# Kernel optimization log

Measured on AMD Instinct MI355X. Metric: run time of the kernel, lower is better.

Reference implementation:

```python
import jax, jax.numpy as jnp
import numpy as np

L, C, K, D = 100000, 20000, 10000, 64   # learners, courses, concepts, feat dim (post-MLP 64)
E_UC, E_UK, E_CK = 1_500_000, 2_000_000, 200_000
LAYERS = 2
EPS = 1e-8


def _sym_laplace_bipartite(key, n_a, n_b, n_edges):
    """Random bipartite graph -> symmetric (n_a+n_b) COO with Laplace normalization,
    matching laplace_transform(): 1/(sqrt(rowsum)+eps) * A * 1/(sqrt(colsum)+eps)."""
    ka, kb = jax.random.split(key)
    a = jax.random.randint(ka, (n_edges,), 0, n_a)
    b = jax.random.randint(kb, (n_edges,), 0, n_b)
    ones = jnp.ones((n_edges,), jnp.float32)
    deg_a = jax.ops.segment_sum(ones, a, num_segments=n_a)
    deg_b = jax.ops.segment_sum(ones, b, num_segments=n_b)
    v = 1.0 / (jnp.sqrt(deg_a[a]) + EPS) / (jnp.sqrt(deg_b[b]) + EPS)
    rows = jnp.concatenate([a, b + n_a]).astype(jnp.int32)
    cols = jnp.concatenate([b + n_a, a]).astype(jnp.int32)
    vals = jnp.concatenate([v, v]).astype(jnp.float32)
    return rows, cols, vals


def setup_inputs() -> dict:
    key = jax.random.key(0)
    k1, k2, k3, k4, k5, k6 = jax.random.split(key, 6)
    cg_rows, cg_cols, cg_vals = _sym_laplace_bipartite(k1, L, C, E_UC)
    kg_rows, kg_cols, kg_vals = _sym_laplace_bipartite(k2, L, K, E_UK)
    # course-concept aggregation graph: row-normalized diag(1/(rowsum+eps)) @ G
    kc, kk = jax.random.split(k3)
    c = jax.random.randint(kc, (E_CK,), 0, C)
    k_ = jax.random.randint(kk, (E_CK,), 0, K)
    deg_c = jax.ops.segment_sum(jnp.ones((E_CK,), jnp.float32), c, num_segments=C)
    ca_vals = (1.0 / (deg_c + EPS))[c].astype(jnp.float32)
    return {
        "learners_feature": jax.random.normal(k4, (L, D), jnp.float32),
        "courses_feature": jax.random.normal(k5, (C, D), jnp.float32),
        "concepts_feature": jax.random.normal(k6, (K, D), jnp.float32),
        "cg_rows": cg_rows, "cg_cols": cg_cols, "cg_vals": cg_vals,
        "kg_rows": kg_rows, "kg_cols": kg_cols, "kg_vals": kg_vals,
        "ca_rows": c.astype(jnp.int32), "ca_cols": k_.astype(jnp.int32), "ca_vals": ca_vals,
    }


def _spmm(rows, cols, vals, feat, n_out):
    # sparse COO (n_out x n_in) @ dense (n_in x D): gather + weighted scatter-add
    return jax.ops.segment_sum(vals[:, None] * feat[cols], rows, num_segments=n_out)


def _l2norm(x):
    # F.normalize(p=2, dim=1) with eps clamp
    n = jnp.linalg.norm(x, axis=1, keepdims=True)
    return x / jnp.maximum(n, 1e-12)


def _graph_propagate(rows, cols, vals, A, B):
    feat = jnp.concatenate([A, B], axis=0)
    n = feat.shape[0]
    acc = feat  # layer-0 features (un-normalized, as in original all_features[0])
    for i in range(LAYERS):
        feat = _spmm(rows, cols, vals, feat, n) / (i + 2)
        acc = acc + _l2norm(feat)
    return acc[: A.shape[0]], acc[A.shape[0]:]


def reference(learners_feature, courses_feature, concepts_feature,
              cg_rows, cg_cols, cg_vals,
              kg_rows, kg_cols, kg_vals,
              ca_rows, ca_cols, ca_vals):
    # course-grained view: propagate over learner-course graph
    cg_l, cg_c = _graph_propagate(cg_rows, cg_cols, cg_vals, learners_feature, courses_feature)
    # concept-grained view: propagate over learner-concept graph
    kg_l, kg_k = _graph_propagate(kg_rows, kg_cols, kg_vals, learners_feature, concepts_feature)
    # aggregate concept-grained concept features into course representations
    kg_c = _spmm(ca_rows, ca_cols, ca_vals, kg_k, courses_feature.shape[0])
    learners_rep = cg_l + kg_l            # [L, D]
    courses_rep = cg_c + kg_c             # [C, D]
    return jnp.concatenate([learners_rep, courses_rep], axis=0)  # [L+C, D]
```

## Files before the change

### kernel.cpp

```cpp
#include <hip/hip_runtime.h>

#define D 64
#define S0 10
#define BCHUNK 8

#define BKT_CNTCG 0
#define BKT_CNTKG 256
#define BKT_BASECG 512
#define BKT_BASEKG 772
#define BKT_CURCG 1032
#define BKT_CURKG 1288
#define BKT_WORDS 2048

__device__ __forceinline__ unsigned int f2bf(float x) {
  unsigned int u = __float_as_uint(x);
  return (u + 0x7FFFu + ((u >> 16) & 1u)) >> 16;
}


__global__ __launch_bounds__(256) void axcopy_kernel(float* __restrict__ dst,
                                                     const float* __restrict__ src,
                                                     long long n4, float s) {
  long long i = (long long)blockIdx.x * blockDim.x + threadIdx.x;
  long long stride = (long long)gridDim.x * blockDim.x;
  for (; i < n4; i += stride) {
    float4 v = ((const float4*)src)[i];
    v.x *= s; v.y *= s; v.z *= s; v.w *= s;
    ((float4*)dst)[i] = v;
  }
}


__global__ __launch_bounds__(1024) void bincnt_kernel(
    const int* __restrict__ cgr, const int* __restrict__ cgc, long long EcgH,
    const int* __restrict__ kgr, const int* __restrict__ kgc, long long EkgH,
    const int* __restrict__ car, long long Eca,
    int* __restrict__ bkt, int* __restrict__ cadeg,
    int L, int NB0, int s1cg, int s1kg) {
  __shared__ int h[512];
  int t = threadIdx.x;
  if (t < 512) h[t] = 0;
  __syncthreads();
  long long i = (long long)blockIdx.x * blockDim.x + t;
  long long stride = (long long)gridDim.x * blockDim.x;
  long long t01 = EcgH + EkgH, tot = t01 + Eca;
  for (; i < tot; i += stride) {
    if (i < EcgH) {
      int a = cgr[i], c = cgc[i];
      atomicAdd(&h[a >> S0], 1);
      atomicAdd(&h[NB0 + ((c - L) >> s1cg)], 1);
    } else if (i < t01) {
      long long j = i - EcgH;
      int a = kgr[j], c = kgc[j];
      atomicAdd(&h[256 + (a >> S0)], 1);
      atomicAdd(&h[256 + NB0 + ((c - L) >> s1kg)], 1);
    } else {
      long long j = i - t01;
      atomicAdd(&cadeg[car[j]], 1);
    }
  }
  __syncthreads();
  if (t < 512 && h[t]) atomicAdd(&bkt[t], h[t]);
}

__global__ __launch_bounds__(256) void bktscan_kernel(int* __restrict__ bkt,
                                                      int NBcg, int NBkg) {
  __shared__ int lds[256];
  int t = threadIdx.x;
  #pragma unroll
  for (int g = 0; g < 2; ++g) {
    int NB      = g ? NBkg : NBcg;
    int cntoff  = g ? BKT_CNTKG : BKT_CNTCG;
    int baseoff = g ? BKT_BASEKG : BKT_BASECG;
    int curoff  = g ? BKT_CURKG : BKT_CURCG;
    lds[t] = (t < NB) ? bkt[cntoff + t] : 0;
    __syncthreads();
    for (int off = 1; off < 256; off <<= 1) {
      int x = (t >= off) ? lds[t - off] : 0;
      __syncthreads();
      lds[t] += x;
      __syncthreads();
    }
    int excl = (t == 0) ? 0 : lds[t - 1];
    if (t < NB) { bkt[baseoff + t] = excl; bkt[curoff + t] = excl; }
    if (t == NB - 1) bkt[baseoff + NB] = lds[t];
    __syncthreads();
  }
}

__global__ __launch_bounds__(256) void ca_scan1_kernel(const int* __restrict__ deg,
                                                       int* __restrict__ rp,
                                                       float* __restrict__ scal,
                                                       int* __restrict__ part, int n) {
  __shared__ int lds[256];
  int b = blockIdx.x, t = threadIdx.x;
  int base = b * 1024 + t * 4;
  int v[4]; int s = 0;
  #pragma unroll
  for (int j = 0; j < 4; j++) {
    int idx = base + j;
    v[j] = (idx < n) ? deg[idx] : 0;
    if (idx < n) scal[idx] = 1.0f / ((float)v[j] + 1e-8f);
    s += v[j];
  }
  lds[t] = s;
  __syncthreads();
  for (int off = 1; off < 256; off <<= 1) {
    int x = (t >= off) ? lds[t - off] : 0;
    __syncthreads();
    lds[t] += x;
    __syncthreads();
  }
  int run = (t == 0) ? 0 : lds[t - 1];
  if (t == 255) part[b] = lds[255];
  #pragma unroll
  for (int j = 0; j < 4; j++) { int idx = base + j; if (idx < n) rp[idx] = run; run += v[j]; }
}

__global__ __launch_bounds__(256) void ca_scan2_kernel(int* __restrict__ part, int nb) {
  __shared__ int lds[256];
  int t = threadIdx.x;
  lds[t] = (t < nb) ? part[t] : 0;
  __syncthreads();
  for (int off = 1; off < 256; off <<= 1) {
    int x = (t >= off) ? lds[t - off] : 0;
    __syncthreads();
    lds[t] += x;
    __syncthreads();
  }
  if (t < nb) part[t] = (t == 0) ? 0 : lds[t - 1];
}

__global__ __launch_bounds__(256) void ca_scan3_kernel(int* __restrict__ rp,
                                                       const int* __restrict__ part,
                                                       int* __restrict__ cacur,
                                                       int n, int total) {
  int b = blockIdx.x, t = threadIdx.x;
  int add = part[b];
  int base = b * 1024 + t * 4;
  #pragma unroll
  for (int j = 0; j < 4; j++) {
    int idx = base + j;
    if (idx < n) { int f = rp[idx] + add; rp[idx] = f; cacur[idx] = f; }
  }
  if (b == 0 && t == 0) rp[n] = total;
}

__global__ __launch_bounds__(256) void bin_kernel(
    const int* __restrict__ rowsA, const int* __restrict__ colsA, long long E,
    int L, int s1, int NB0, int NBtot,
    int* __restrict__ gcur, int* __restrict__ binned) {
  __shared__ int cnt[256];
  __shared__ int gbase[256];
  int t = threadIdx.x;
  long long base = (long long)blockIdx.x * (256 * BCHUNK);
  cnt[t] = 0;
  __syncthreads();
  int av[BCHUNK], cv_[BCHUNK], l0[BCHUNK], l1[BCHUNK];
  #pragma unroll
  for (int k = 0; k < BCHUNK; k++) {
    long long i = base + (long long)k * 256 + t;
    bool ok = i < E;
    int a = ok ? rowsA[i] : 0;
    int c = ok ? colsA[i] : L;
    av[k] = a; cv_[k] = c;
    if (ok) {
      int b0 = a >> S0;
      int b1 = NB0 + ((c - L) >> s1);
      l0[k] = atomicAdd(&cnt[b0], 1);
      l1[k] = atomicAdd(&cnt[b1], 1);
    } else { l0[k] = 0; l1[k] = 0; }
  }
  __syncthreads();
  if (t < NBtot) gbase[t] = cnt[t] ? atomicAdd(&gcur[t], cnt[t]) : 0;
  __syncthreads();
  #pragma unroll
  for (int k = 0; k < BCHUNK; k++) {
    long long i = base + (long long)k * 256 + t;
    if (i < E) {
      int a = av[k], c = cv_[k];
      int b0 = a >> S0;
      int b1 = NB0 + ((c - L) >> s1);
      binned[gbase[b0] + l0[k]] = ((a & ((1 << S0) - 1)) << 17) | c;
      binned[gbase[b1] + l1[k]] = (((c - L) & ((1 << s1) - 1)) << 17) | a;
    }
  }
}

__global__ __launch_bounds__(1024) void fine2_kernel(
    const int* __restrict__ binned, const int* __restrict__ bktbase,
    int* __restrict__ rp, int* __restrict__ cvout, float* __restrict__ scal,
    int L, int sideEnd, int s1, int NB0, int nfull) {
  __shared__ int cnt[1 << S0];
  int b = blockIdx.x, t = threadIdx.x;
  int rowbase, rowend;
  if (b < NB0) { rowbase = b << S0; rowend = min(rowbase + (1 << S0), L); }
  else { int bb = b - NB0; rowbase = L + (bb << s1); rowend = min(rowbase + (1 << s1), sideEnd); }
  int nrows = rowend - rowbase;
  int base = bktbase[b], end = bktbase[b + 1];
  cnt[t] = 0;
  __syncthreads();
  for (int i = base + t; i < end; i += 1024) atomicAdd(&cnt[binned[i] >> 17], 1);
  __syncthreads();
  int deg = cnt[t];
  for (int off = 1; off < 1024; off <<= 1) {
    int x = (t >= off) ? cnt[t - off] : 0;
    __syncthreads();
    cnt[t] += x;
    __syncthreads();
  }
  int excl = (t == 0) ? 0 : cnt[t - 1];
  int pos = base + excl;
  __syncthreads();
  cnt[t] = pos;
  if (t < nrows) {
    rp[rowbase + t] = pos;
    scal[rowbase + t] = 1.0f / (sqrtf((float)deg) + 1e-8f);
  }
  if (b == gridDim.x - 1 && t == 0) rp[nfull] = end;
  __syncthreads();
  for (int i = base + t; i < end; i += 1024) {
    int w = binned[i];
    int p = atomicAdd(&cnt[w >> 17], 1);
    cvout[p] = w & 0x1FFFF;
  }
}

__global__ __launch_bounds__(256) void scatter_ca_kernel(
    const int* __restrict__ rows, const int* __restrict__ cols,
    int* __restrict__ rowcur, int* __restrict__ cv, long long ne) {
  long long e = (long long)blockIdx.x * blockDim.x + threadIdx.x;
  if (e >= ne) return;
  int p = atomicAdd(&rowcur[rows[e]], 1);
  cv[p] = cols[e];
}

__global__ __launch_bounds__(256) void cvt_all_kernel(
    const float* __restrict__ learners, const float* __restrict__ courses,
    const float* __restrict__ concepts, const float* __restrict__ scal,
    unsigned short* __restrict__ g0, int Lr, int Ncg, int Rtot) {
  long long q = (long long)blockIdx.x * blockDim.x + threadIdx.x;
  long long stride = (long long)gridDim.x * blockDim.x;
  long long nq = (long long)Rtot * 16;
  for (; q < nq; q += stride) {
    int row = (int)(q >> 4);
    int sub = ((int)q & 15) * 4;
    const float* src;
    if (row < Ncg) src = (row < Lr) ? learners + (long long)row * D
                                    : courses + (long long)(row - Lr) * D;
    else {
      int r = row - Ncg;
      src = (r < Lr) ? learners + (long long)r * D
                     : concepts + (long long)(r - Lr) * D;
    }
    float sg = scal[row];
    float4 v = *(const float4*)(src + sub);
    unsigned int lo = f2bf(v.x * sg) | (f2bf(v.y * sg) << 16);
    unsigned int hi = f2bf(v.z * sg) | (f2bf(v.w * sg) << 16);
    *(uint2*)(g0 + (long long)row * D + sub) = make_uint2(lo, hi);
  }
}

template <int MODE, int INITA, int INITB>
__global__ __launch_bounds__(256) void pull4_kernel(
    const int* __restrict__ rowptr, const int* __restrict__ cols,
    const unsigned short* __restrict__ gt, unsigned short* __restrict__ g1,
    const float* __restrict__ sigRow,
    float* __restrict__ accA, float* __restrict__ accB, int splitAcc,
    const float* __restrict__ i0A, const float* __restrict__ i0B, int i0Split,
    float i0ScaleA, float i0ScaleB, int nrows) {
  int row = blockIdx.x * 4 + (threadIdx.x >> 6);
  if (row >= nrows) return;
  int lane = threadIdx.x & 63;
  int sub = lane & 15;
  int grp = lane >> 4;
  int e0 = rowptr[row], e1 = rowptr[row + 1];
  float sx = 0.f, sy = 0.f, sz = 0.f, sw = 0.f;
  long long dimoff = (long long)(sub << 2);
  int e = e0;
  for (; e + 16 <= e1; e += 16) {
    int c0 = cols[e + grp];
    int c1 = cols[e + 4 + grp];
    int c2 = cols[e + 8 + grp];
    int c3 = cols[e + 12 + grp];
    uint2 v0 = *(const uint2*)(gt + ((long long)c0 << 6) + dimoff);
    uint2 v1 = *(const uint2*)(gt + ((long long)c1 << 6) + dimoff);
    uint2 v2 = *(const uint2*)(gt + ((long long)c2 << 6) + dimoff);
    uint2 v3 = *(const uint2*)(gt + ((long long)c3 << 6) + dimoff);
    sx += __uint_as_float(v0.x << 16);
    sy += __uint_as_float(v0.x & 0xFFFF0000u);
    sz += __uint_as_float(v0.y << 16);
    sw += __uint_as_float(v0.y & 0xFFFF0000u);
    sx += __uint_as_float(v1.x << 16);
    sy += __uint_as_float(v1.x & 0xFFFF0000u);
    sz += __uint_as_float(v1.y << 16);
    sw += __uint_as_float(v1.y & 0xFFFF0000u);
    sx += __uint_as_float(v2.x << 16);
    sy += __uint_as_float(v2.x & 0xFFFF0000u);
    sz += __uint_as_float(v2.y << 16);
    sw += __uint_as_float(v2.y & 0xFFFF0000u);
    sx += __uint_as_float(v3.x << 16);
    sy += __uint_as_float(v3.x & 0xFFFF0000u);
    sz += __uint_as_float(v3.y << 16);
    sw += __uint_as_float(v3.y & 0xFFFF0000u);
  }
  for (int ee = e + grp; ee < e1; ee += 4) {
    int c = cols[ee];
    uint2 v = *(const uint2*)(gt + ((long long)c << 6) + dimoff);
    sx += __uint_as_float(v.x << 16);
    sy += __uint_as_float(v.x & 0xFFFF0000u);
    sz += __uint_as_float(v.y << 16);
    sw += __uint_as_float(v.y & 0xFFFF0000u);
  }
  #pragma unroll
  for (int off = 16; off <= 32; off <<= 1) {
    sx += __shfl_xor(sx, off);
    sy += __shfl_xor(sy, off);
    sz += __shfl_xor(sz, off);
    sw += __shfl_xor(sw, off);
  }
  float q = sx * sx + sy * sy + sz * sz + sw * sw;
  #pragma unroll
  for (int off = 1; off <= 8; off <<= 1) q += __shfl_xor(q, off);
  float r = 1.0f / fmaxf(sqrtf(q), 1e-12f);

  if (grp == 0) {
    long long off4 = dimoff;
    if (MODE == 0) {
      float sg = sigRow[row];
      float f = sg * sg;
      unsigned int lo = f2bf(f * sx) | (f2bf(f * sy) << 16);
      unsigned int hi = f2bf(f * sz) | (f2bf(f * sw) << 16);
      *(uint2*)(g1 + ((long long)row << 6) + (sub << 2)) = make_uint2(lo, hi);
    }
    float4 base;
    float* dst;
    if (row < splitAcc) {
      dst = accA + ((long long)row << 6);
      if (INITA) {
        bool lo_ = row < i0Split;
        const float* src = lo_ ? i0A + ((long long)row << 6)
                               : i0B + ((long long)(row - i0Split) << 6);
        float sc = lo_ ? i0ScaleA : i0ScaleB;
        float4 v = *(const float4*)(src + off4);
        base = make_float4(sc * v.x, sc * v.y, sc * v.z, sc * v.w);
      } else base = *(const float4*)(dst + off4);
    } else {
      dst = accB + ((long long)(row - splitAcc) << 6);
      if (INITB) {
        const float* src = i0B + ((long long)(row - i0Split) << 6);
        float4 v = *(const float4*)(src + off4);
        base = make_float4(i0ScaleB * v.x, i0ScaleB * v.y, i0ScaleB * v.z, i0ScaleB * v.w);
      } else base = *(const float4*)(dst + off4);
    }
    *(float4*)(dst + off4) = make_float4(base.x + sx * r, base.y + sy * r,
                                         base.z + sz * r, base.w + sw * r);
  }
}

__global__ __launch_bounds__(256) void pull_ca_kernel(
    const int* __restrict__ rowptr, const int* __restrict__ cols,
    const float* __restrict__ invdeg, const float* __restrict__ feat,
    float* __restrict__ acc, int nrows) {
  int row = blockIdx.x * 4 + (threadIdx.x >> 6);
  if (row >= nrows) return;
  int lane = threadIdx.x & 63;
  int e0 = rowptr[row], e1 = rowptr[row + 1];
  float s = 0.f;
  for (int e = e0; e < e1; ++e) s += feat[((long long)cols[e] << 6) + lane];
  acc[((long long)row << 6) + lane] += invdeg[row] * s;
}


__global__ __launch_bounds__(256) void spmm_atomic_kernel(
    const int* __restrict__ rows, const int* __restrict__ cols,
    const float* __restrict__ vals, const float* __restrict__ feat,
    float* __restrict__ outp, long long ne) {
  long long t = (long long)blockIdx.x * blockDim.x + threadIdx.x;
  long long e = t >> 4;
  if (e >= ne) return;
  int lane = (int)(t & 15);
  int r = rows[e];
  int c = cols[e];
  float v = vals[e];
  const float4 f = *(const float4*)(feat + (long long)c * D + lane * 4);
  float* o = outp + (long long)r * D + lane * 4;
  atomicAdd(o + 0, v * f.x);
  atomicAdd(o + 1, v * f.y);
  atomicAdd(o + 2, v * f.z);
  atomicAdd(o + 3, v * f.w);
}

__global__ __launch_bounds__(256) void norm_acc_kernel(const float* __restrict__ feat,
                                                       float* __restrict__ acc,
                                                       int nrows) {
  int row = blockIdx.x * 4 + (threadIdx.x >> 6);
  if (row >= nrows) return;
  int lane = threadIdx.x & 63;
  float x = feat[(long long)row * D + lane];
  float s = x * x;
  #pragma unroll
  for (int off = 32; off; off >>= 1) s += __shfl_xor(s, off);
  float sc = 1.0f / fmaxf(sqrtf(s), 1e-12f);
  acc[(long long)row * D + lane] += x * sc;
}


extern "C" void kernel_launch(void* const* d_in, const int* in_sizes, int n_in,
                              void* d_out, int out_size, void* d_ws, size_t ws_size,
                              hipStream_t stream) {
  const float* learners = (const float*)d_in[0];
  const float* courses  = (const float*)d_in[1];
  const float* concepts = (const float*)d_in[2];
  const int*   cg_rows  = (const int*)d_in[3];
  const int*   cg_cols  = (const int*)d_in[4];
  const int*   kg_rows  = (const int*)d_in[6];
  const int*   kg_cols  = (const int*)d_in[7];
  const int*   ca_rows  = (const int*)d_in[9];
  const int*   ca_cols  = (const int*)d_in[10];
  const float* cg_vals  = (const float*)d_in[5];
  const float* kg_vals  = (const float*)d_in[8];
  const float* ca_vals  = (const float*)d_in[11];

  const long long Lr  = in_sizes[0] / D;
  const long long Cr  = in_sizes[1] / D;
  const long long Kr  = in_sizes[2] / D;
  const long long Ecg = in_sizes[3];
  const long long Ekg = in_sizes[6];
  const long long Eca = in_sizes[9];
  const long long EcgH = Ecg / 2;
  const long long EkgH = Ekg / 2;
  const long long Ncg = Lr + Cr;
  const long long Nkg = Lr + Kr;

  float* out = (float*)d_out;

  const int NB0   = (int)((Lr + (1 << S0) - 1) >> S0);
  const int s1cg  = 8;
  const int s1kg  = 6;
  const int NBcg  = NB0 + (int)((Cr + (1 << s1cg) - 1) >> s1cg);
  const int NBkg  = NB0 + (int)((Kr + (1 << s1kg) - 1) >> s1kg);

  long long maxE = (Ecg > Ekg ? Ecg : Ekg);
  long long maxN = (Ncg > Nkg ? Ncg : Nkg);
  long long shareW = maxE > maxN * 32 ? maxE : maxN * 32;
  size_t need = 0;
  auto walloc = [&](long long elems) { size_t off = need; need += ((size_t)elems + 3) & ~(size_t)3; return off; };
  int* wsbase = (int*)d_ws;
  size_t o_share = walloc(shareW);
  size_t o_g0    = walloc((Ncg + Nkg) * 32);
  size_t o_acck  = walloc(Kr * D);
  size_t o_rp0   = walloc(Ncg + 1);
  size_t o_rp1   = walloc(Nkg + 1);
  size_t o_rp2   = walloc(Cr + 1);
  size_t o_cv0   = walloc(Ecg);
  size_t o_cv1   = walloc(Ekg);
  size_t o_cv2   = walloc(Eca);
  size_t o_bkt   = walloc(BKT_WORDS);
  size_t o_cadeg = walloc(Cr);
  size_t o_scal  = walloc(Ncg + Nkg + Cr);
  size_t o_part  = walloc(512);
  size_t o_cacur = walloc(Cr);

  auto axcopy = [&](float* dst, const float* src, long long n, float s) {
    long long n4 = n / 4;
    long long b = (n4 + 255) / 256;
    int blocks = (int)(b < 2048 ? b : 2048);
    axcopy_kernel<<<blocks, 256, 0, stream>>>(dst, src, n4, s);
  };

  bool packable = (Ncg <= 131072) && (Nkg <= 131072) &&
                  (NBcg <= 256) && (NBkg <= 256) &&
                  (Ecg % 2 == 0) && (Ekg % 2 == 0);
  if (need * 4 > ws_size || !packable) {
    float* buf0 = (float*)d_ws;
    float* buf1 = buf0 + Ncg * D;
    float* acck = buf1 + Ncg * D;
    auto spmm = [&](const int* r, const int* c, const float* v, const float* f,
                    float* o, long long ne) {
      long long threads = ne * 16;
      int blocks = (int)((threads + 255) / 256);
      spmm_atomic_kernel<<<blocks, 256, 0, stream>>>(r, c, v, f, o, ne);
    };
    auto normacc = [&](const float* f, float* a, long long nrows) {
      int blocks = (int)((nrows + 3) / 4);
      norm_acc_kernel<<<blocks, 256, 0, stream>>>(f, a, (int)nrows);
    };
    axcopy(buf0, learners, Lr * D, 1.f);
    axcopy(buf0 + Lr * D, courses, Cr * D, 1.f);
    axcopy(out, learners, Lr * D, 2.f);
    axcopy(out + Lr * D, courses, Cr * D, 1.f);
    hipMemsetAsync(buf1, 0, (size_t)(Ncg * D) * sizeof(float), stream);
    spmm(cg_rows, cg_cols, cg_vals, buf0, buf1, Ecg);
    normacc(buf1, out, Ncg);
    hipMemsetAsync(buf0, 0, (size_t)(Ncg * D) * sizeof(float), stream);
    spmm(cg_rows, cg_cols, cg_vals, buf1, buf0, Ecg);
    normacc(buf0, out, Ncg);
    axcopy(buf0, learners, Lr * D, 1.f);
    axcopy(buf0 + Lr * D, concepts, Kr * D, 1.f);
    axcopy(acck, concepts, Kr * D, 1.f);
    hipMemsetAsync(buf1, 0, (size_t)(Nkg * D) * sizeof(float), stream);
    spmm(kg_rows, kg_cols, kg_vals, buf0, buf1, Ekg);
    normacc(buf1, out, Lr);
    normacc(buf1 + Lr * D, acck, Kr);
    hipMemsetAsync(buf0, 0, (size_t)(Nkg * D) * sizeof(float), stream);
    spmm(kg_rows, kg_cols, kg_vals, buf1, buf0, Ekg);
    normacc(buf0, out, Lr);
    normacc(buf0 + Lr * D, acck, Kr);
    spmm(ca_rows, ca_cols, ca_vals, acck, out + Lr * D, Eca);
    return;
  }

  int*            binned = wsbase + o_share;
  unsigned short* g1     = (unsigned short*)(wsbase + o_share);
  unsigned short* g0     = (unsigned short*)(wsbase + o_g0);
  float* acck   = (float*)(wsbase + o_acck);
  int*   rp0    = wsbase + o_rp0;
  int*   rp1    = wsbase + o_rp1;
  int*   rp2    = wsbase + o_rp2;
  int*   cv0    = wsbase + o_cv0;
  int*   cv1    = wsbase + o_cv1;
  int*   cv2    = wsbase + o_cv2;
  int*   bkt    = wsbase + o_bkt;
  int*   cadeg  = wsbase + o_cadeg;
  float* scal   = (float*)(wsbase + o_scal);
  int*   part   = wsbase + o_part;
  int*   cacur  = wsbase + o_cacur;

  hipMemsetAsync(bkt, 0, (size_t)(BKT_WORDS + ((Cr + 3) & ~3LL)) * sizeof(int), stream);
  bincnt_kernel<<<512, 1024, 0, stream>>>(cg_rows, cg_cols, EcgH, kg_rows, kg_cols, EkgH,
                                          ca_rows, Eca, bkt, cadeg,
                                          (int)Lr, NB0, s1cg, s1kg);
  bktscan_kernel<<<1, 256, 0, stream>>>(bkt, NBcg, NBkg);

  const int nbca = (int)((Cr + 1023) / 1024);
  ca_scan1_kernel<<<nbca, 256, 0, stream>>>(cadeg, rp2, scal + Ncg + Nkg, part, (int)Cr);
  ca_scan2_kernel<<<1, 256, 0, stream>>>(part, nbca);
  ca_scan3_kernel<<<nbca, 256, 0, stream>>>(rp2, part, cacur, (int)Cr, (int)Eca);

  {
    int blocks = (int)((EcgH + 256 * BCHUNK - 1) / (256 * BCHUNK));
    bin_kernel<<<blocks, 256, 0, stream>>>(cg_rows, cg_cols, EcgH, (int)Lr, s1cg, NB0, NBcg,
                                           bkt + BKT_CURCG, binned);
    fine2_kernel<<<NBcg, 1024, 0, stream>>>(binned, bkt + BKT_BASECG, rp0, cv0, scal,
                                            (int)Lr, (int)Ncg, s1cg, NB0, (int)Ncg);
  }
  {
    int blocks = (int)((EkgH + 256 * BCHUNK - 1) / (256 * BCHUNK));
    bin_kernel<<<blocks, 256, 0, stream>>>(kg_rows, kg_cols, EkgH, (int)Lr, s1kg, NB0, NBkg,
                                           bkt + BKT_CURKG, binned);
    fine2_kernel<<<NBkg, 1024, 0, stream>>>(binned, bkt + BKT_BASEKG, rp1, cv1, scal + Ncg,
                                            (int)Lr, (int)Nkg, s1kg, NB0, (int)Nkg);
  }
  scatter_ca_kernel<<<(int)((Eca + 255) / 256), 256, 0, stream>>>(ca_rows, ca_cols, cacur, cv2, Eca);

  cvt_all_kernel<<<4096, 256, 0, stream>>>(learners, courses, concepts, scal,
                                           g0, (int)Lr, (int)Ncg, (int)(Ncg + Nkg));

  const unsigned short* g0cg = g0;
  const unsigned short* g0kg = g0 + (long long)Ncg * D;
  const float* sig_cg = scal;
  const float* sig_kg = scal + Ncg;
  const float* inv_ca = scal + Ncg + Nkg;

  {
    int blocks = (int)((Ncg + 3) / 4);
    pull4_kernel<0, 1, 1><<<blocks, 256, 0, stream>>>(
        rp0, cv0, g0cg, g1, sig_cg,
        out, out, (int)Ncg,
        learners, courses, (int)Lr, 2.0f, 1.0f, (int)Ncg);
    pull4_kernel<1, 0, 0><<<blocks, 256, 0, stream>>>(
        rp0, cv0, g1, nullptr, nullptr,
        out, out, (int)Ncg,
        nullptr, nullptr, 0, 0.f, 0.f, (int)Ncg);
  }

  {
    int blocks = (int)((Nkg + 3) / 4);
    pull4_kernel<0, 0, 1><<<blocks, 256, 0, stream>>>(
        rp1, cv1, g0kg, g1, sig_kg,
        out, acck, (int)Lr,
        nullptr, concepts, (int)Lr, 0.f, 1.0f, (int)Nkg);
    pull4_kernel<1, 0, 0><<<blocks, 256, 0, stream>>>(
        rp1, cv1, g1, nullptr, nullptr,
        out, acck, (int)Lr,
        nullptr, nullptr, 0, 0.f, 0.f, (int)Nkg);
  }

  {
    int blocks = (int)((Cr + 3) / 4);
    pull_ca_kernel<<<blocks, 256, 0, stream>>>(rp2, cv2, inv_ca, acck,
                                               out + Lr * D, (int)Cr);
  }
}
```

Baseline: 660.4 us.

## Bin edges into padded buckets in one pass and fuse CSR build with bf16 conversion

```diff
diff --git a/kernel.cpp b/kernel.cpp
--- a/kernel.cpp
+++ b/kernel.cpp
@@ -3,18 +3,37 @@
 #define D 64
 #define S0 10
 #define BCHUNK 8
-
-#define BKT_CNTCG 0
-#define BKT_CNTKG 256
-#define BKT_BASECG 512
-#define BKT_BASEKG 772
-#define BKT_CURCG 1032
-#define BKT_CURKG 1288
-#define BKT_WORDS 2048
+#define EPB (256 * BCHUNK)
 
 __device__ __forceinline__ unsigned int f2bf(float x) {
   unsigned int u = __float_as_uint(x);
   return (u + 0x7FFFu + ((u >> 16) & 1u)) >> 16;
+}
+
+
+struct BP {
+  const int *cgr, *cgc, *kgr, *kgc, *car;
+  long long EcgH, EkgH, Eca, Ecg, Ekg;
+  int Bcg, Bkg;
+  int L, Ncg, Nkg, NB0, NBcg, NBkg, s1cg, s1kg;
+  int capcg0, capcg1, capkg0, capkg1;
+  long long padcg;
+  int *gcur;
+  int *bkt;
+  int *cadeg;
+  int *binned;
+  int *rp0, *rp1, *cv0, *cv1;
+  float *scal;
+  unsigned short *g0;
+  const float *learners, *courses, *concepts;
+};
+
+__device__ __forceinline__ long long rbase(const BP& P, int g, int b) {
+  if (g == 0)
+    return b < P.NB0 ? (long long)b * P.capcg0
+                     : (long long)P.NB0 * P.capcg0 + (long long)(b - P.NB0) * P.capcg1;
+  return P.padcg + (b < P.NB0 ? (long long)b * P.capkg0
+                              : (long long)P.NB0 * P.capkg0 + (long long)(b - P.NB0) * P.capkg1);
 }
 
 
@@ -31,49 +50,76 @@
 }
 
 
-__global__ __launch_bounds__(1024) void bincnt_kernel(
-    const int* __restrict__ cgr, const int* __restrict__ cgc, long long EcgH,
-    const int* __restrict__ kgr, const int* __restrict__ kgc, long long EkgH,
-    const int* __restrict__ car, long long Eca,
-    int* __restrict__ bkt, int* __restrict__ cadeg,
-    int L, int NB0, int s1cg, int s1kg) {
-  __shared__ int h[512];
+__global__ __launch_bounds__(512) void init_gcur_kernel(BP P) {
   int t = threadIdx.x;
-  if (t < 512) h[t] = 0;
-  __syncthreads();
-  long long i = (long long)blockIdx.x * blockDim.x + t;
-  long long stride = (long long)gridDim.x * blockDim.x;
-  long long t01 = EcgH + EkgH, tot = t01 + Eca;
-  for (; i < tot; i += stride) {
-    if (i < EcgH) {
-      int a = cgr[i], c = cgc[i];
-      atomicAdd(&h[a >> S0], 1);
-      atomicAdd(&h[NB0 + ((c - L) >> s1cg)], 1);
-    } else if (i < t01) {
-      long long j = i - EcgH;
-      int a = kgr[j], c = kgc[j];
-      atomicAdd(&h[256 + (a >> S0)], 1);
-      atomicAdd(&h[256 + NB0 + ((c - L) >> s1kg)], 1);
-    } else {
-      long long j = i - t01;
-      atomicAdd(&cadeg[car[j]], 1);
+  if (t < 256) {
+    if (t < P.NBcg) P.gcur[t] = (int)rbase(P, 0, t);
+  } else {
+    int b = t - 256;
+    if (b < P.NBkg) P.gcur[256 + b] = (int)rbase(P, 1, b);
+  }
+}
+
+__global__ __launch_bounds__(256) void binD_all_kernel(BP P) {
+  int B = blockIdx.x;
+  int t = threadIdx.x;
+  if (B >= P.Bcg + P.Bkg) {
+    long long base = (long long)(B - P.Bcg - P.Bkg) * EPB;
+    #pragma unroll
+    for (int k = 0; k < BCHUNK; k++) {
+      long long i = base + (long long)k * 256 + t;
+      if (i < P.Eca) atomicAdd(&P.cadeg[P.car[i]], 1);
     }
-  }
-  __syncthreads();
-  if (t < 512 && h[t]) atomicAdd(&bkt[t], h[t]);
-}
-
-__global__ __launch_bounds__(256) void bktscan_kernel(int* __restrict__ bkt,
-                                                      int NBcg, int NBkg) {
+    return;
+  }
+  const int* rowsA; const int* colsA; long long E; int s1, NBtot, goff; long long eb;
+  if (B < P.Bcg) { rowsA = P.cgr; colsA = P.cgc; E = P.EcgH; s1 = P.s1cg; NBtot = P.NBcg; goff = 0;   eb = (long long)B * EPB; }
+  else           { rowsA = P.kgr; colsA = P.kgc; E = P.EkgH; s1 = P.s1kg; NBtot = P.NBkg; goff = 256; eb = (long long)(B - P.Bcg) * EPB; }
+
+  __shared__ int cnt[256];
+  __shared__ int gbase[256];
+  cnt[t] = 0;
+  __syncthreads();
+  int av[BCHUNK], cv_[BCHUNK], l0[BCHUNK], l1[BCHUNK];
+  #pragma unroll
+  for (int k = 0; k < BCHUNK; k++) {
+    long long i = eb + (long long)k * 256 + t;
+    bool ok = i < E;
+    int a = ok ? rowsA[i] : 0;
+    int c = ok ? colsA[i] : P.L;
+    av[k] = a; cv_[k] = c;
+    if (ok) {
+      int b0 = a >> S0;
+      int b1 = P.NB0 + ((c - P.L) >> s1);
+      l0[k] = atomicAdd(&cnt[b0], 1);
+      l1[k] = atomicAdd(&cnt[b1], 1);
+    } else { l0[k] = 0; l1[k] = 0; }
+  }
+  __syncthreads();
+  if (t < NBtot) gbase[t] = cnt[t] ? atomicAdd(&P.gcur[goff + t], cnt[t]) : 0;
+  __syncthreads();
+  #pragma unroll
+  for (int k = 0; k < BCHUNK; k++) {
+    long long i = eb + (long long)k * 256 + t;
+    if (i < E) {
+      int a = av[k], c = cv_[k];
+      int b0 = a >> S0;
+      int b1 = P.NB0 + ((c - P.L) >> s1);
+      P.binned[gbase[b0] + l0[k]] = ((a & ((1 << S0) - 1)) << 17) | c;
+      P.binned[gbase[b1] + l1[k]] = (((c - P.L) & ((1 << s1) - 1)) << 17) | a;
+    }
+  }
+}
+
+__global__ __launch_bounds__(256) void scan_all_kernel(BP P) {
   __shared__ int lds[256];
   int t = threadIdx.x;
   #pragma unroll
   for (int g = 0; g < 2; ++g) {
-    int NB      = g ? NBkg : NBcg;
-    int cntoff  = g ? BKT_CNTKG : BKT_CNTCG;
-    int baseoff = g ? BKT_BASEKG : BKT_BASECG;
-    int curoff  = g ? BKT_CURKG : BKT_CURCG;
-    lds[t] = (t < NB) ? bkt[cntoff + t] : 0;
+    int NB = g ? P.NBkg : P.NBcg;
+    int c = 0;
+    if (t < NB) c = P.gcur[g * 256 + t] - (int)rbase(P, g, t);
+    lds[t] = c;
     __syncthreads();
     for (int off = 1; off < 256; off <<= 1) {
       int x = (t >= off) ? lds[t - off] : 0;
@@ -81,11 +127,10 @@
       lds[t] += x;
       __syncthreads();
     }
-    int excl = (t == 0) ? 0 : lds[t - 1];
-    if (t < NB) { bkt[baseoff + t] = excl; bkt[curoff + t] = excl; }
-    if (t == NB - 1) bkt[baseoff + NB] = lds[t];
+    if (t < NB) P.bkt[g * 256 + t] = (t == 0) ? 0 : lds[t - 1];
     __syncthreads();
   }
+  if (t == 0) { P.rp0[P.Ncg] = (int)P.Ecg; P.rp1[P.Nkg] = (int)P.Ekg; }
 }
 
 __global__ __launch_bounds__(256) void ca_scan1_kernel(const int* __restrict__ deg,
@@ -146,83 +191,67 @@
   if (b == 0 && t == 0) rp[n] = total;
 }
 
-__global__ __launch_bounds__(256) void bin_kernel(
-    const int* __restrict__ rowsA, const int* __restrict__ colsA, long long E,
-    int L, int s1, int NB0, int NBtot,
-    int* __restrict__ gcur, int* __restrict__ binned) {
-  __shared__ int cnt[256];
-  __shared__ int gbase[256];
-  int t = threadIdx.x;
-  long long base = (long long)blockIdx.x * (256 * BCHUNK);
+__global__ __launch_bounds__(1024) void fine3_all_kernel(BP P) {
+  __shared__ int cnt[1 << S0];
+  __shared__ int wsum[16];
+  int B = blockIdx.x, t = threadIdx.x;
+  int g = (B < P.NBcg) ? 0 : 1;
+  int lb = g ? B - P.NBcg : B;
+  int s1 = g ? P.s1kg : P.s1cg;
+  int sideEnd = g ? P.Nkg : P.Ncg;
+  int* rp = g ? P.rp1 : P.rp0;
+  int* cv = g ? P.cv1 : P.cv0;
+  float* scal = P.scal + (g ? P.Ncg : 0);
+  long long g0off = g ? (long long)P.Ncg : 0;
+  const float* fB = g ? P.concepts : P.courses;
+
+  int rowbase, rowend;
+  if (lb < P.NB0) { rowbase = lb << S0; rowend = min(rowbase + (1 << S0), P.L); }
+  else { int bb = lb - P.NB0; rowbase = P.L + (bb << s1); rowend = min(rowbase + (1 << s1), sideEnd); }
+  int nrows = rowend - rowbase;
+  long long base = rbase(P, g, lb);
+  int count = P.gcur[g * 256 + lb] - (int)base;
+  int csrbase = P.bkt[g * 256 + lb];
+
   cnt[t] = 0;
   __syncthreads();
-  int av[BCHUNK], cv_[BCHUNK], l0[BCHUNK], l1[BCHUNK];
-  #pragma unroll
-  for (int k = 0; k < BCHUNK; k++) {
-    long long i = base + (long long)k * 256 + t;
-    bool ok = i < E;
-    int a = ok ? rowsA[i] : 0;
-    int c = ok ? colsA[i] : L;
-    av[k] = a; cv_[k] = c;
-    if (ok) {
-      int b0 = a >> S0;
-      int b1 = NB0 + ((c - L) >> s1);
-      l0[k] = atomicAdd(&cnt[b0], 1);
-      l1[k] = atomicAdd(&cnt[b1], 1);
-    } else { l0[k] = 0; l1[k] = 0; }
-  }
-  __syncthreads();
-  if (t < NBtot) gbase[t] = cnt[t] ? atomicAdd(&gcur[t], cnt[t]) : 0;
-  __syncthreads();
-  #pragma unroll
-  for (int k = 0; k < BCHUNK; k++) {
-    long long i = base + (long long)k * 256 + t;
-    if (i < E) {
-      int a = av[k], c = cv_[k];
-      int b0 = a >> S0;
-      int b1 = NB0 + ((c - L) >> s1);
-      binned[gbase[b0] + l0[k]] = ((a & ((1 << S0) - 1)) << 17) | c;
-      binned[gbase[b1] + l1[k]] = (((c - L) & ((1 << s1) - 1)) << 17) | a;
-    }
-  }
-}
-
-__global__ __launch_bounds__(1024) void fine2_kernel(
-    const int* __restrict__ binned, const int* __restrict__ bktbase,
-    int* __restrict__ rp, int* __restrict__ cvout, float* __restrict__ scal,
-    int L, int sideEnd, int s1, int NB0, int nfull) {
-  __shared__ int cnt[1 << S0];
-  int b = blockIdx.x, t = threadIdx.x;
-  int rowbase, rowend;
-  if (b < NB0) { rowbase = b << S0; rowend = min(rowbase + (1 << S0), L); }
-  else { int bb = b - NB0; rowbase = L + (bb << s1); rowend = min(rowbase + (1 << s1), sideEnd); }
-  int nrows = rowend - rowbase;
-  int base = bktbase[b], end = bktbase[b + 1];
-  cnt[t] = 0;
-  __syncthreads();
-  for (int i = base + t; i < end; i += 1024) atomicAdd(&cnt[binned[i] >> 17], 1);
+  for (int i = t; i < count; i += 1024) atomicAdd(&cnt[P.binned[base + i] >> 17], 1);
   __syncthreads();
   int deg = cnt[t];
-  for (int off = 1; off < 1024; off <<= 1) {
-    int x = (t >= off) ? cnt[t - off] : 0;
-    __syncthreads();
-    cnt[t] += x;
-    __syncthreads();
-  }
-  int excl = (t == 0) ? 0 : cnt[t - 1];
-  int pos = base + excl;
-  __syncthreads();
+  int lane = t & 63, wid = t >> 6;
+  int v = deg;
+  #pragma unroll
+  for (int off = 1; off < 64; off <<= 1) {
+    int y = __shfl_up(v, off);
+    if (lane >= off) v += y;
+  }
+  if (lane == 63) wsum[wid] = v;
+  __syncthreads();
+  if (t == 0) { int run = 0; for (int w = 0; w < 16; w++) { int x = wsum[w]; wsum[w] = run; run += x; } }
+  __syncthreads();
+  int pos = csrbase + wsum[wid] + (v - deg);
   cnt[t] = pos;
   if (t < nrows) {
-    rp[rowbase + t] = pos;
-    scal[rowbase + t] = 1.0f / (sqrtf((float)deg) + 1e-8f);
-  }
-  if (b == gridDim.x - 1 && t == 0) rp[nfull] = end;
-  __syncthreads();
-  for (int i = base + t; i < end; i += 1024) {
-    int w = binned[i];
+    int row = rowbase + t;
+    rp[row] = pos;
+    float sg = 1.0f / (sqrtf((float)deg) + 1e-8f);
+    scal[row] = sg;
+    const float* src = row < P.L ? P.learners + (long long)row * D
+                                 : fB + (long long)(row - P.L) * D;
+    unsigned short* gdst = P.g0 + (g0off + row) * D;
+    #pragma unroll 4
+    for (int q = 0; q < 16; q++) {
+      float4 x = *(const float4*)(src + q * 4);
+      unsigned int lo = f2bf(x.x * sg) | (f2bf(x.y * sg) << 16);
+      unsigned int hi = f2bf(x.z * sg) | (f2bf(x.w * sg) << 16);
+      *(uint2*)(gdst + q * 4) = make_uint2(lo, hi);
+    }
+  }
+  __syncthreads();
+  for (int i = t; i < count; i += 1024) {
+    int w = P.binned[base + i];
     int p = atomicAdd(&cnt[w >> 17], 1);
-    cvout[p] = w & 0x1FFFF;
+    cv[p] = w & 0x1FFFF;
   }
 }
 
@@ -233,32 +262,6 @@
   if (e >= ne) return;
   int p = atomicAdd(&rowcur[rows[e]], 1);
   cv[p] = cols[e];
-}
-
-__global__ __launch_bounds__(256) void cvt_all_kernel(
-    const float* __restrict__ learners, const float* __restrict__ courses,
-    const float* __restrict__ concepts, const float* __restrict__ scal,
-    unsigned short* __restrict__ g0, int Lr, int Ncg, int Rtot) {
-  long long q = (long long)blockIdx.x * blockDim.x + threadIdx.x;
-  long long stride = (long long)gridDim.x * blockDim.x;
-  long long nq = (long long)Rtot * 16;
-  for (; q < nq; q += stride) {
-    int row = (int)(q >> 4);
-    int sub = ((int)q & 15) * 4;
-    const float* src;
-    if (row < Ncg) src = (row < Lr) ? learners + (long long)row * D
-                                    : courses + (long long)(row - Lr) * D;
-    else {
-      int r = row - Ncg;
-      src = (r < Lr) ? learners + (long long)r * D
-                     : concepts + (long long)(r - Lr) * D;
-    }
-    float sg = scal[row];
-    float4 v = *(const float4*)(src + sub);
-    unsigned int lo = f2bf(v.x * sg) | (f2bf(v.y * sg) << 16);
-    unsigned int hi = f2bf(v.z * sg) | (f2bf(v.w * sg) << 16);
-    *(uint2*)(g0 + (long long)row * D + sub) = make_uint2(lo, hi);
-  }
 }
 
 template <int MODE, int INITA, int INITB>
@@ -438,12 +441,21 @@
   const int NB0   = (int)((Lr + (1 << S0) - 1) >> S0);
   const int s1cg  = 8;
   const int s1kg  = 6;
-  const int NBcg  = NB0 + (int)((Cr + (1 << s1cg) - 1) >> s1cg);
-  const int NBkg  = NB0 + (int)((Kr + (1 << s1kg) - 1) >> s1kg);
-
-  long long maxE = (Ecg > Ekg ? Ecg : Ekg);
+  const int NB1cg = (int)((Cr + (1 << s1cg) - 1) >> s1cg);
+  const int NB1kg = (int)((Kr + (1 << s1kg) - 1) >> s1kg);
+  const int NBcg  = NB0 + NB1cg;
+  const int NBkg  = NB0 + NB1kg;
+
+  const int capcg0 = 2 * (int)((EcgH + NB0 - 1) / NB0);
+  const int capcg1 = 2 * (int)((EcgH + NB1cg - 1) / NB1cg);
+  const int capkg0 = 2 * (int)((EkgH + NB0 - 1) / NB0);
+  const int capkg1 = 2 * (int)((EkgH + NB1kg - 1) / NB1kg);
+  const long long padcg = (long long)NB0 * capcg0 + (long long)NB1cg * capcg1;
+  const long long padkg = (long long)NB0 * capkg0 + (long long)NB1kg * capkg1;
+  const long long padtot = padcg + padkg;
+
   long long maxN = (Ncg > Nkg ? Ncg : Nkg);
-  long long shareW = maxE > maxN * 32 ? maxE : maxN * 32;
+  long long shareW = padtot > maxN * 32 ? padtot : maxN * 32;
   size_t need = 0;
   auto walloc = [&](long long elems) { size_t off = need; need += ((size_t)elems + 3) & ~(size_t)3; return off; };
   int* wsbase = (int*)d_ws;
@@ -456,7 +468,8 @@
   size_t o_cv0   = walloc(Ecg);
   size_t o_cv1   = walloc(Ekg);
   size_t o_cv2   = walloc(Eca);
-  size_t o_bkt   = walloc(BKT_WORDS);
+  size_t o_gcur  = walloc(512);
+  size_t o_bkt   = walloc(512);
   size_t o_cadeg = walloc(Cr);
   size_t o_scal  = walloc(Ncg + Nkg + Cr);
   size_t o_part  = walloc(512);
@@ -471,7 +484,7 @@
 
   bool packable = (Ncg <= 131072) && (Nkg <= 131072) &&
                   (NBcg <= 256) && (NBkg <= 256) &&
-                  (Ecg % 2 == 0) && (Ekg % 2 == 0);
+                  (Ecg % 2 == 0) && (Ekg % 2 == 0) && (Lr >= 1);
   if (need * 4 > ws_size || !packable) {
     float* buf0 = (float*)d_ws;
     float* buf1 = buf0 + Ncg * D;
@@ -521,41 +534,41 @@
   int*   cv0    = wsbase + o_cv0;
   int*   cv1    = wsbase + o_cv1;
   int*   cv2    = wsbase + o_cv2;
+  int*   gcur   = wsbase + o_gcur;
   int*   bkt    = wsbase + o_bkt;
   int*   cadeg  = wsbase + o_cadeg;
   float* scal   = (float*)(wsbase + o_scal);
   int*   part   = wsbase + o_part;
   int*   cacur  = wsbase + o_cacur;
 
-  hipMemsetAsync(bkt, 0, (size_t)(BKT_WORDS + ((Cr + 3) & ~3LL)) * sizeof(int), stream);
-  bincnt_kernel<<<512, 1024, 0, stream>>>(cg_rows, cg_cols, EcgH, kg_rows, kg_cols, EkgH,
-                                          ca_rows, Eca, bkt, cadeg,
-                                          (int)Lr, NB0, s1cg, s1kg);
-  bktscan_kernel<<<1, 256, 0, stream>>>(bkt, NBcg, NBkg);
+  BP P;
+  P.cgr = cg_rows; P.cgc = cg_cols; P.kgr = kg_rows; P.kgc = kg_cols; P.car = ca_rows;
+  P.EcgH = EcgH; P.EkgH = EkgH; P.Eca = Eca; P.Ecg = Ecg; P.Ekg = Ekg;
+  P.Bcg = (int)((EcgH + EPB - 1) / EPB);
+  P.Bkg = (int)((EkgH + EPB - 1) / EPB);
+  P.L = (int)Lr; P.Ncg = (int)Ncg; P.Nkg = (int)Nkg;
+  P.NB0 = NB0; P.NBcg = NBcg; P.NBkg = NBkg; P.s1cg = s1cg; P.s1kg = s1kg;
+  P.capcg0 = capcg0; P.capcg1 = capcg1; P.capkg0 = capkg0; P.capkg1 = capkg1;
+  P.padcg = padcg;
+  P.gcur = gcur; P.bkt = bkt; P.cadeg = cadeg; P.binned = binned;
+  P.rp0 = rp0; P.rp1 = rp1; P.cv0 = cv0; P.cv1 = cv1;
+  P.scal = scal; P.g0 = g0;
+  P.learners = learners; P.courses = courses; P.concepts = concepts;
+
+  const int Bca = (int)((Eca + EPB - 1) / EPB);
+
+  hipMemsetAsync(cadeg, 0, (size_t)Cr * sizeof(int), stream);
+  init_gcur_kernel<<<1, 512, 0, stream>>>(P);
+  binD_all_kernel<<<P.Bcg + P.Bkg + Bca, 256, 0, stream>>>(P);
+  scan_all_kernel<<<1, 256, 0, stream>>>(P);
 
   const int nbca = (int)((Cr + 1023) / 1024);
   ca_scan1_kernel<<<nbca, 256, 0, stream>>>(cadeg, rp2, scal + Ncg + Nkg, part, (int)Cr);
   ca_scan2_kernel<<<1, 256, 0, stream>>>(part, nbca);
   ca_scan3_kernel<<<nbca, 256, 0, stream>>>(rp2, part, cacur, (int)Cr, (int)Eca);
 
-  {
-    int blocks = (int)((EcgH + 256 * BCHUNK - 1) / (256 * BCHUNK));
-    bin_kernel<<<blocks, 256, 0, stream>>>(cg_rows, cg_cols, EcgH, (int)Lr, s1cg, NB0, NBcg,
-                                           bkt + BKT_CURCG, binned);
-    fine2_kernel<<<NBcg, 1024, 0, stream>>>(binned, bkt + BKT_BASECG, rp0, cv0, scal,
-                                            (int)Lr, (int)Ncg, s1cg, NB0, (int)Ncg);
-  }
-  {
-    int blocks = (int)((EkgH + 256 * BCHUNK - 1) / (256 * BCHUNK));
-    bin_kernel<<<blocks, 256, 0, stream>>>(kg_rows, kg_cols, EkgH, (int)Lr, s1kg, NB0, NBkg,
-                                           bkt + BKT_CURKG, binned);
-    fine2_kernel<<<NBkg, 1024, 0, stream>>>(binned, bkt + BKT_BASEKG, rp1, cv1, scal + Ncg,
-                                            (int)Lr, (int)Nkg, s1kg, NB0, (int)Nkg);
-  }
+  fine3_all_kernel<<<NBcg + NBkg, 1024, 0, stream>>>(P);
   scatter_ca_kernel<<<(int)((Eca + 255) / 256), 256, 0, stream>>>(ca_rows, ca_cols, cacur, cv2, Eca);
-
-  cvt_all_kernel<<<4096, 256, 0, stream>>>(learners, courses, concepts, scal,
-                                           g0, (int)Lr, (int)Ncg, (int)(Ncg + Nkg));
 
   const unsigned short* g0cg = g0;
   const unsigned short* g0kg = g0 + (long long)Ncg * D;
```

Result: slower. 718.5 us (+8.8%).

## Fuse bf16 feature conversion into fine2 and use wave-shuffle prefix scan

Applied to the files above, without the earlier changes.

```diff
diff --git a/kernel.cpp b/kernel.cpp
--- a/kernel.cpp
+++ b/kernel.cpp
@@ -190,8 +190,11 @@
 __global__ __launch_bounds__(1024) void fine2_kernel(
     const int* __restrict__ binned, const int* __restrict__ bktbase,
     int* __restrict__ rp, int* __restrict__ cvout, float* __restrict__ scal,
+    const float* __restrict__ fA, const float* __restrict__ fB,
+    unsigned short* __restrict__ g0g,
     int L, int sideEnd, int s1, int NB0, int nfull) {
   __shared__ int cnt[1 << S0];
+  __shared__ int wsum[16];
   int b = blockIdx.x, t = threadIdx.x;
   int rowbase, rowend;
   if (b < NB0) { rowbase = b << S0; rowend = min(rowbase + (1 << S0), L); }
@@ -203,15 +206,18 @@
   for (int i = base + t; i < end; i += 1024) atomicAdd(&cnt[binned[i] >> 17], 1);
   __syncthreads();
   int deg = cnt[t];
-  for (int off = 1; off < 1024; off <<= 1) {
-    int x = (t >= off) ? cnt[t - off] : 0;
-    __syncthreads();
-    cnt[t] += x;
-    __syncthreads();
-  }
-  int excl = (t == 0) ? 0 : cnt[t - 1];
-  int pos = base + excl;
-  __syncthreads();
+  int lane = t & 63, wid = t >> 6;
+  int v = deg;
+  #pragma unroll
+  for (int off = 1; off < 64; off <<= 1) {
+    int y = __shfl_up(v, off);
+    if (lane >= off) v += y;
+  }
+  if (lane == 63) wsum[wid] = v;
+  __syncthreads();
+  if (t == 0) { int run = 0; for (int w = 0; w < 16; w++) { int x = wsum[w]; wsum[w] = run; run += x; } }
+  __syncthreads();
+  int pos = base + wsum[wid] + (v - deg);
   cnt[t] = pos;
   if (t < nrows) {
     rp[rowbase + t] = pos;
@@ -219,6 +225,19 @@
   }
   if (b == gridDim.x - 1 && t == 0) rp[nfull] = end;
   __syncthreads();
+
+  for (int r0 = wid * 4 + (lane >> 4); r0 < nrows; r0 += 64) {
+    int row = rowbase + r0;
+    float sg = scal[row];
+    int sub = lane & 15;
+    const float* src = (row < L ? fA + (long long)row * D
+                                : fB + (long long)(row - L) * D) + sub * 4;
+    float4 x = *(const float4*)src;
+    unsigned int lo = f2bf(x.x * sg) | (f2bf(x.y * sg) << 16);
+    unsigned int hi = f2bf(x.z * sg) | (f2bf(x.w * sg) << 16);
+    *(uint2*)(g0g + (long long)row * D + sub * 4) = make_uint2(lo, hi);
+  }
+
   for (int i = base + t; i < end; i += 1024) {
     int w = binned[i];
     int p = atomicAdd(&cnt[w >> 17], 1);
@@ -233,32 +252,6 @@
   if (e >= ne) return;
   int p = atomicAdd(&rowcur[rows[e]], 1);
   cv[p] = cols[e];
-}
-
-__global__ __launch_bounds__(256) void cvt_all_kernel(
-    const float* __restrict__ learners, const float* __restrict__ courses,
-    const float* __restrict__ concepts, const float* __restrict__ scal,
-    unsigned short* __restrict__ g0, int Lr, int Ncg, int Rtot) {
-  long long q = (long long)blockIdx.x * blockDim.x + threadIdx.x;
-  long long stride = (long long)gridDim.x * blockDim.x;
-  long long nq = (long long)Rtot * 16;
-  for (; q < nq; q += stride) {
-    int row = (int)(q >> 4);
-    int sub = ((int)q & 15) * 4;
-    const float* src;
-    if (row < Ncg) src = (row < Lr) ? learners + (long long)row * D
-                                    : courses + (long long)(row - Lr) * D;
-    else {
-      int r = row - Ncg;
-      src = (r < Lr) ? learners + (long long)r * D
-                     : concepts + (long long)(r - Lr) * D;
-    }
-    float sg = scal[row];
-    float4 v = *(const float4*)(src + sub);
-    unsigned int lo = f2bf(v.x * sg) | (f2bf(v.y * sg) << 16);
-    unsigned int hi = f2bf(v.z * sg) | (f2bf(v.w * sg) << 16);
-    *(uint2*)(g0 + (long long)row * D + sub) = make_uint2(lo, hi);
-  }
 }
 
 template <int MODE, int INITA, int INITB>
@@ -543,6 +536,7 @@
     bin_kernel<<<blocks, 256, 0, stream>>>(cg_rows, cg_cols, EcgH, (int)Lr, s1cg, NB0, NBcg,
                                            bkt + BKT_CURCG, binned);
     fine2_kernel<<<NBcg, 1024, 0, stream>>>(binned, bkt + BKT_BASECG, rp0, cv0, scal,
+                                            learners, courses, g0,
                                             (int)Lr, (int)Ncg, s1cg, NB0, (int)Ncg);
   }
   {
@@ -550,12 +544,10 @@
     bin_kernel<<<blocks, 256, 0, stream>>>(kg_rows, kg_cols, EkgH, (int)Lr, s1kg, NB0, NBkg,
                                            bkt + BKT_CURKG, binned);
     fine2_kernel<<<NBkg, 1024, 0, stream>>>(binned, bkt + BKT_BASEKG, rp1, cv1, scal + Ncg,
+                                            learners, concepts, g0 + (long long)Ncg * D,
                                             (int)Lr, (int)Nkg, s1kg, NB0, (int)Nkg);
   }
   scatter_ca_kernel<<<(int)((Eca + 255) / 256), 256, 0, stream>>>(ca_rows, ca_cols, cacur, cv2, Eca);
-
-  cvt_all_kernel<<<4096, 256, 0, stream>>>(learners, courses, concepts, scal,
-                                           g0, (int)Lr, (int)Ncg, (int)(Ncg + Nkg));
 
   const unsigned short* g0cg = g0;
   const unsigned short* g0kg = g0 + (long long)Ncg * D;
```

New measurement: 665.4 us. Within noise of the previous version (+0.8%).
